# Kernel optimization log

Measured on AMD Instinct MI355X. Metric: run time of the kernel, lower is better.

Reference implementation:

```python
import jax, jax.numpy as jnp
import numpy as np

B, N, D = 8, 1024, 1024

def setup_inputs() -> dict:
    key = jax.random.key(0)
    k1, k2, k3, k4, k5 = jax.random.split(key, 5)
    x = jax.random.normal(k1, (B, N, D), dtype=jnp.float32)
    y = jax.random.normal(k2, (B, N, D), dtype=jnp.float32)
    adj = jax.random.uniform(k3, (B, N, N), dtype=jnp.float32)
    adj_sumrow = jnp.sum(adj, axis=-1, keepdims=True)  # [B, N, 1], row-sum normalizer
    W = jax.random.normal(k4, (D, D), dtype=jnp.float32) * (1.0 / np.sqrt(D))
    b = jax.random.normal(k5, (D,), dtype=jnp.float32) * 0.02
    return {"x": x, "y": y, "adj": adj, "adj_sumrow": adj_sumrow, "W": W, "b": b}

def reference(x, y, adj, adj_sumrow, W, b):
    # GraphConvolutionCustom: project neighbor features, aggregate via dense adj,
    # normalize by row-sum, add bias and residual input x; then ReLU.
    # Dropout is identity in eval mode (training=False).
    support = jnp.einsum('bnd,de->bne', y, W)          # [B, N, D]
    agg = jnp.matmul(adj, support) / adj_sumrow        # [B, N, D]
    out = jax.nn.relu(agg + b + x)
    return out
```

## Files before the change

kernel.cpp:

```cpp
#include <hip/hip_runtime.h>
#include <hip/hip_bf16.h>
#include <stdint.h>


typedef float  f32x4  __attribute__((ext_vector_type(4)));
typedef __bf16 bf16x8 __attribute__((ext_vector_type(8)));

__device__ __forceinline__ unsigned short f2bf(float f) {
  union { float f; unsigned int u; } c; c.f = f;
  unsigned int u = c.u;
  u += 0x7FFFu + ((u >> 16) & 1u);
  return (unsigned short)(u >> 16);
}

__device__ __forceinline__ void async_cp16(const void* g, void* l) {
  __builtin_amdgcn_global_load_lds(
      (const __attribute__((address_space(1))) unsigned int*)g,
      (__attribute__((address_space(3))) unsigned int*)l, 16, 0, 0);
}

__device__ __forceinline__ void bar() { asm volatile("s_barrier" ::: "memory"); }


__global__ __launch_bounds__(256) void k_prep(
    const float4* __restrict__ y4, const float4* __restrict__ a4,
    ushort4* __restrict__ yb, ushort4* __restrict__ ab,
    const float* __restrict__ W, unsigned short* __restrict__ Wt)
{
  __shared__ float t[64][65];
  const int bid = blockIdx.x;
  if (bid < 16384) {
    const int i = bid * 256 + threadIdx.x;
    const bool isY = i < 2097152;
    const float4 v = isY ? y4[i] : a4[i - 2097152];
    ushort4 p;
    p.x = f2bf(v.x); p.y = f2bf(v.y); p.z = f2bf(v.z); p.w = f2bf(v.w);
    if (isY) yb[i] = p; else ab[i - 2097152] = p;
  } else {
    const int id = bid - 16384;
    const int n0 = (id & 15) * 64, k0 = (id >> 4) * 64;
    const int tx = threadIdx.x & 63, ty = threadIdx.x >> 6;
#pragma unroll
    for (int r = ty; r < 64; r += 4)
      t[r][tx] = W[(size_t)(k0 + r) * 1024 + n0 + tx];
    __syncthreads();
#pragma unroll
    for (int r = ty; r < 64; r += 4)
      Wt[(size_t)(n0 + r) * 1024 + k0 + tx] = f2bf(t[tx][r]);
  }
}


__device__ __forceinline__ void stage512(
    const unsigned short* __restrict__ A,  int sA,
    const unsigned short* __restrict__ Bt, int sB,
    int m0, int n0, int k0,
    unsigned short* la, unsigned short* lb,
    int wave, int rg, int colo)
{
#pragma unroll
  for (int s = 0; s < 2; ++s) {
    const int t = wave * 2 + s;
    async_cp16(A  + (size_t)(m0 + t * 8 + rg) * sA + k0 + colo, la + t * 512);
    async_cp16(Bt + (size_t)(n0 + t * 8 + rg) * sB + k0 + colo, lb + t * 512);
  }
}

__device__ __forceinline__ void compute512(
    const unsigned short* la, const unsigned short* lb,
    f32x4 acc[2][4], int wm, int wn, int quad, int l16)
{
#pragma unroll
  for (int h = 0; h < 2; ++h) {
    bf16x8 af[2], bfr[4];
#pragma unroll
    for (int i = 0; i < 2; ++i) {
      const int r = wm + i * 16 + l16;
      af[i] = *(const bf16x8*)(la + r * 64 + ((h * 4 + quad + r) & 7) * 8);
    }
#pragma unroll
    for (int j = 0; j < 4; ++j) {
      const int r = wn + j * 16 + l16;
      bfr[j] = *(const bf16x8*)(lb + r * 64 + ((h * 4 + quad + r) & 7) * 8);
    }
#pragma unroll
    for (int i = 0; i < 2; ++i)
#pragma unroll
      for (int j = 0; j < 4; ++j)
        acc[i][j] = __builtin_amdgcn_mfma_f32_16x16x32_bf16(af[i], bfr[j], acc[i][j], 0, 0, 0);
  }
}

__device__ __forceinline__ void gemm_dbuf(
    const unsigned short* __restrict__ A,  int sA,
    const unsigned short* __restrict__ Bt, int sB,
    int m0, int n0, f32x4 acc[2][4], unsigned short* lsm, int tid)
{
  const int lane = tid & 63, wave = tid >> 6;
  const int wm = (wave >> 1) * 32, wn = (wave & 1) * 64;
  const int quad = lane >> 4, l16 = lane & 15;
  const int rg = lane >> 3;
  const int colo = (((lane & 7) - rg) & 7) * 8;
  unsigned short* la0 = lsm;
  unsigned short* lb0 = lsm + 8192;
  unsigned short* la1 = lsm + 16384;
  unsigned short* lb1 = lsm + 24576;

  stage512(A, sA, Bt, sB, m0, n0, 0, la0, lb0, wave, rg, colo);
#pragma unroll 1
  for (int k0 = 0; k0 < 1024; k0 += 128) {
    stage512(A, sA, Bt, sB, m0, n0, k0 + 64, la1, lb1, wave, rg, colo);
    asm volatile("s_waitcnt vmcnt(4)" ::: "memory");
    bar();
    compute512(la0, lb0, acc, wm, wn, quad, l16);
    bar();
    if (k0 + 128 < 1024) {
      stage512(A, sA, Bt, sB, m0, n0, k0 + 128, la0, lb0, wave, rg, colo);
      asm volatile("s_waitcnt vmcnt(4)" ::: "memory");
    } else {
      asm volatile("s_waitcnt vmcnt(0)" ::: "memory");
    }
    bar();
    compute512(la1, lb1, acc, wm, wn, quad, l16);
    bar();
  }
}

__device__ __forceinline__ void zero_acc(f32x4 acc[2][4]) {
#pragma unroll
  for (int i = 0; i < 2; ++i)
#pragma unroll
    for (int j = 0; j < 4; ++j)
#pragma unroll
      for (int r = 0; r < 4; ++r) acc[i][j][r] = 0.0f;
}


__global__ __launch_bounds__(512, 4) void k_gemm1(
    const unsigned short* __restrict__ Wt,
    const unsigned short* __restrict__ Ybf,
    unsigned short* __restrict__ Sup2)
{
  __shared__ __align__(16) unsigned short lsm[4 * 8192];
  const int tid = threadIdx.x;
  const int n0 = blockIdx.x * 128, m0 = blockIdx.y * 128;

  f32x4 acc[2][4];
  zero_acc(acc);
  gemm_dbuf(Wt, 1024, Ybf, 1024, m0, n0, acc, lsm, tid);

  const int lane = tid & 63, wave = tid >> 6;
  const int wm = (wave >> 1) * 32, wn = (wave & 1) * 64;
  const int quad = lane >> 4, l16 = lane & 15;
#pragma unroll
  for (int i = 0; i < 2; ++i) {
    const int mb = m0 + wm + i * 16 + quad * 4;
#pragma unroll
    for (int r = 0; r < 4; ++r) {
      unsigned short* row = Sup2 + ((size_t)(mb + r) << 13);
#pragma unroll
      for (int j = 0; j < 4; ++j)
        row[n0 + wn + j * 16 + l16] = f2bf(acc[i][j][r]);
    }
  }
}


__global__ __launch_bounds__(512, 4) void k_gemm2(
    const unsigned short* __restrict__ AdjBf,
    const unsigned short* __restrict__ Sup2,
    const float* __restrict__ x,
    const float* __restrict__ sumrow,
    const float* __restrict__ bias,
    float* __restrict__ out)
{
  __shared__ __align__(16) unsigned short lsm[4 * 8192];
  const int tid = threadIdx.x;
  const int n0 = blockIdx.x * 128, m0 = blockIdx.y * 128, b = blockIdx.z;

  f32x4 acc[2][4];
  zero_acc(acc);
  gemm_dbuf(AdjBf + ((size_t)b << 20), 1024,
            Sup2 + ((size_t)b << 10), 8192,
            m0, n0, acc, lsm, tid);

  const float* xb = x   + ((size_t)b << 20);
  float*       ob = out + ((size_t)b << 20);
  const float* sr = sumrow + ((size_t)b << 10);
  const int lane = tid & 63, wave = tid >> 6;
  const int wm = (wave >> 1) * 32, wn = (wave & 1) * 64;
  const int quad = lane >> 4, l16 = lane & 15;

  float bv[4];
#pragma unroll
  for (int j = 0; j < 4; ++j) bv[j] = bias[n0 + wn + j * 16 + l16];

#pragma unroll
  for (int i = 0; i < 2; ++i) {
    const int mb = m0 + wm + i * 16 + quad * 4;
#pragma unroll
    for (int r = 0; r < 4; ++r) {
      const int m = mb + r;
      const float inv = 1.0f / sr[m];
#pragma unroll
      for (int j = 0; j < 4; ++j) {
        const int n = n0 + wn + j * 16 + l16;
        const size_t idx = (((size_t)m) << 10) + n;
        float v = acc[i][j][r] * inv + bv[j] + xb[idx];
        ob[idx] = fmaxf(v, 0.0f);
      }
    }
  }
}


extern "C" void kernel_launch(void* const* d_in, const int* in_sizes, int n_in,
                              void* d_out, int out_size, void* d_ws, size_t ws_size,
                              hipStream_t stream) {
  const float* x      = (const float*)d_in[0];
  const float* y      = (const float*)d_in[1];
  const float* adj    = (const float*)d_in[2];
  const float* sumrow = (const float*)d_in[3];
  const float* W      = (const float*)d_in[4];
  const float* bias   = (const float*)d_in[5];
  float* out = (float*)d_out;

  char* ws = (char*)d_ws;
  unsigned short* ybf   = (unsigned short*)(ws);
  unsigned short* adjbf = (unsigned short*)(ws + ((size_t)16 << 20));
  unsigned short* wt    = (unsigned short*)(ws + ((size_t)32 << 20));
  unsigned short* sup2  = (unsigned short*)(ws + ((size_t)34 << 20));

  k_prep<<<dim3(16640), dim3(256), 0, stream>>>(
      (const float4*)y, (const float4*)adj, (ushort4*)ybf, (ushort4*)adjbf, W, wt);
  k_gemm1<<<dim3(64, 8), dim3(512), 0, stream>>>(wt, ybf, sup2);
  k_gemm2<<<dim3(8, 8, 8), dim3(512), 0, stream>>>(adjbf, sup2, x, sumrow, bias, out);
}
```

Measured before the change: 196.7 us.

## Deepen GEMM pipeline to four LDS stages and remap blocks for XCD locality

Replaces the double-buffered K loop with a four-stage ring of LDS buffers that prefetches three 64-wide K tiles ahead, using vmcnt waits, so global loads are more hidden behind MFMA work. LDS per block doubles to 128KB and launch bounds drop to 2 blocks per CU. Both GEMMs now use a 1D grid with a swizzled block-to-tile mapping so consecutive blocks on the same XCD share A/B tiles in L2. The larger LDS footprint lowers occupancy.

```diff
diff --git a/kernel.cpp b/kernel.cpp
--- a/kernel.cpp
+++ b/kernel.cpp
@@ -91,7 +91,7 @@
   }
 }
 
-__device__ __forceinline__ void gemm_dbuf(
+__device__ __forceinline__ void gemm_quad(
     const unsigned short* __restrict__ A,  int sA,
     const unsigned short* __restrict__ Bt, int sB,
     int m0, int n0, f32x4 acc[2][4], unsigned short* lsm, int tid)
@@ -101,27 +101,27 @@
   const int quad = lane >> 4, l16 = lane & 15;
   const int rg = lane >> 3;
   const int colo = (((lane & 7) - rg) & 7) * 8;
-  unsigned short* la0 = lsm;
-  unsigned short* lb0 = lsm + 8192;
-  unsigned short* la1 = lsm + 16384;
-  unsigned short* lb1 = lsm + 24576;
-
-  stage512(A, sA, Bt, sB, m0, n0, 0, la0, lb0, wave, rg, colo);
-#pragma unroll 1
-  for (int k0 = 0; k0 < 1024; k0 += 128) {
-    stage512(A, sA, Bt, sB, m0, n0, k0 + 64, la1, lb1, wave, rg, colo);
-    asm volatile("s_waitcnt vmcnt(4)" ::: "memory");
-    bar();
-    compute512(la0, lb0, acc, wm, wn, quad, l16);
-    bar();
-    if (k0 + 128 < 1024) {
-      stage512(A, sA, Bt, sB, m0, n0, k0 + 128, la0, lb0, wave, rg, colo);
+
+  stage512(A, sA, Bt, sB, m0, n0, 0,   lsm,           lsm + 8192,          wave, rg, colo);
+  stage512(A, sA, Bt, sB, m0, n0, 64,  lsm + 16384,   lsm + 16384 + 8192,  wave, rg, colo);
+  stage512(A, sA, Bt, sB, m0, n0, 128, lsm + 32768,   lsm + 32768 + 8192,  wave, rg, colo);
+
+#pragma unroll
+  for (int k = 0; k < 16; ++k) {
+    if (k < 13) {
+      unsigned short* base = lsm + ((k + 3) & 3) * 16384;
+      stage512(A, sA, Bt, sB, m0, n0, (k + 3) * 64, base, base + 8192, wave, rg, colo);
+      asm volatile("s_waitcnt vmcnt(12)" ::: "memory");
+    } else if (k == 13) {
+      asm volatile("s_waitcnt vmcnt(8)" ::: "memory");
+    } else if (k == 14) {
       asm volatile("s_waitcnt vmcnt(4)" ::: "memory");
     } else {
       asm volatile("s_waitcnt vmcnt(0)" ::: "memory");
     }
     bar();
-    compute512(la1, lb1, acc, wm, wn, quad, l16);
+    const unsigned short* cb = lsm + (k & 3) * 16384;
+    compute512(cb, cb + 8192, acc, wm, wn, quad, l16);
     bar();
   }
 }
@@ -136,18 +136,20 @@
 }
 
 
-__global__ __launch_bounds__(512, 4) void k_gemm1(
+__global__ __launch_bounds__(512, 2) void k_gemm1(
     const unsigned short* __restrict__ Wt,
     const unsigned short* __restrict__ Ybf,
     unsigned short* __restrict__ Sup2)
 {
-  __shared__ __align__(16) unsigned short lsm[4 * 8192];
+  __shared__ __align__(16) unsigned short lsm[65536];
   const int tid = threadIdx.x;
-  const int n0 = blockIdx.x * 128, m0 = blockIdx.y * 128;
+  const int bid = blockIdx.x;
+  const int l = ((bid & 7) << 6) | (bid >> 3);
+  const int m0 = (l & 7) << 7, n0 = (l >> 3) << 7;
 
   f32x4 acc[2][4];
   zero_acc(acc);
-  gemm_dbuf(Wt, 1024, Ybf, 1024, m0, n0, acc, lsm, tid);
+  gemm_quad(Wt, 1024, Ybf, 1024, m0, n0, acc, lsm, tid);
 
   const int lane = tid & 63, wave = tid >> 6;
   const int wm = (wave >> 1) * 32, wn = (wave & 1) * 64;
@@ -166,7 +168,7 @@
 }
 
 
-__global__ __launch_bounds__(512, 4) void k_gemm2(
+__global__ __launch_bounds__(512, 2) void k_gemm2(
     const unsigned short* __restrict__ AdjBf,
     const unsigned short* __restrict__ Sup2,
     const float* __restrict__ x,
@@ -174,13 +176,16 @@
     const float* __restrict__ bias,
     float* __restrict__ out)
 {
-  __shared__ __align__(16) unsigned short lsm[4 * 8192];
+  __shared__ __align__(16) unsigned short lsm[65536];
   const int tid = threadIdx.x;
-  const int n0 = blockIdx.x * 128, m0 = blockIdx.y * 128, b = blockIdx.z;
+  const int bid = blockIdx.x;
+  const int l = ((bid & 7) << 6) | (bid >> 3);
+  const int b = l >> 6;
+  const int m0 = ((l >> 3) & 7) << 7, n0 = (l & 7) << 7;
 
   f32x4 acc[2][4];
   zero_acc(acc);
-  gemm_dbuf(AdjBf + ((size_t)b << 20), 1024,
+  gemm_quad(AdjBf + ((size_t)b << 20), 1024,
             Sup2 + ((size_t)b << 10), 8192,
             m0, n0, acc, lsm, tid);
 
@@ -233,6 +238,6 @@
 
   k_prep<<<dim3(16640), dim3(256), 0, stream>>>(
       (const float4*)y, (const float4*)adj, (ushort4*)ybf, (ushort4*)adjbf, W, wt);
-  k_gemm1<<<dim3(64, 8), dim3(512), 0, stream>>>(wt, ybf, sup2);
-  k_gemm2<<<dim3(8, 8, 8), dim3(512), 0, stream>>>(adjbf, sup2, x, sumrow, bias, out);
-}
+  k_gemm1<<<dim3(512), dim3(512), 0, stream>>>(wt, ybf, sup2);
+  k_gemm2<<<dim3(512), dim3(512), 0, stream>>>(adjbf, sup2, x, sumrow, bias, out);
+}
```

Measured after the change: 198.3 us. About the same (+0.8%).
